# Performance work log

Measured on AMD Instinct MI355X. Metric: run time of the kernel, lower is better.

## Reference

```python
import jax, jax.numpy as jnp
import numpy as np


def _conv(x, w, padding):
    # x: NCHW, w: OIHW
    return jax.lax.conv_general_dilated(
        x, w, window_strides=(1, 1), padding=padding,
        dimension_numbers=('NCHW', 'OIHW', 'NCHW'))


def setup_inputs() -> dict:
    key = jax.random.key(0)
    ks = jax.random.split(key, 4)
    B, Cin, H, W = 128, 1024, 14, 14
    planes, expansion = 256, 4
    x = jax.random.normal(ks[0], (B, Cin, H, W), dtype=jnp.float32)
    # conv weights (layouts are fully dense since rho=0.0)
    w1 = jax.random.normal(ks[1], (planes, Cin, 1, 1), dtype=jnp.float32) * 0.02
    w2 = jax.random.normal(ks[2], (planes, planes, 3, 3), dtype=jnp.float32) * 0.02
    w3 = jax.random.normal(ks[3], (planes * expansion, planes, 1, 1), dtype=jnp.float32) * 0.02
    # Fixup scalar biases / scale
    z = jnp.zeros((1,), dtype=jnp.float32)
    return {
        'x': x, 'w1': w1, 'w2': w2, 'w3': w3,
        'bias1b': z, 'bias2a': z, 'bias2b': z, 'bias3a': z, 'bias3b': z,
        'rscale': jnp.ones((1,), dtype=jnp.float32), 'rbias': z,
    }


def reference(x, w1, w2, w3, bias1b, bias2a, bias2b, bias3a, bias3b, rscale, rbias):
    # conv1(x) + bias1b  (1x1, fused output bias)
    out = _conv(x, w1, 'VALID') + bias1b[0]
    # conv2(out + bias2a) + bias2b  (3x3, pad 1, fused input+output bias)
    out = _conv(out + bias2a[0], w2, 'SAME') + bias2b[0]
    # conv3(out + bias3a) + bias3b  (1x1)
    out = _conv(out + bias3a[0], w3, 'VALID') + bias3b[0]
    # fused scale + bias + residual ReLU: relu(out*rscale + rbias + identity)
    return jax.nn.relu(out * rscale[0] + rbias[0] + x)
```

## Files before the change

### kernel.cpp

```cpp
#include <hip/hip_runtime.h>
#include <stdint.h>

typedef __bf16 bf16x8 __attribute__((ext_vector_type(8)));
typedef float f32x4 __attribute__((ext_vector_type(4)));
typedef unsigned short u16;

__device__ __forceinline__ u16 f2bf(float f){
  uint32_t u = __float_as_uint(f);
  u = (u + 0x7fffu + ((u >> 16) & 1u)) >> 16;
  return (u16)u;
}
__device__ __forceinline__ float bf2f(u16 v){
  return __uint_as_float(((uint32_t)v) << 16);
}
__device__ __forceinline__ void gl_lds16(const void* g, void* l){
  __builtin_amdgcn_global_load_lds((const __attribute__((address_space(1))) void*)g,
                                   (__attribute__((address_space(3))) void*)l, 16, 0, 0);
}

__global__ __launch_bounds__(256) void prep_w(
    const float* __restrict__ w1, const float* __restrict__ w2,
    const float* __restrict__ w3, u16* __restrict__ wb1, u16* __restrict__ wb2,
    u16* __restrict__ wb3){
  int bid = blockIdx.x, t = threadIdx.x;
  if (bid < 1024){
    int i = bid*256 + t; wb1[i] = f2bf(w1[i]);
  } else if (bid < 3328){
    int i = (bid-1024)*256 + t;
    int o = i / 2304, r = i - o*2304, kq = r >> 8, c = r & 255;
    wb2[i] = f2bf(w2[((size_t)o*256 + c)*9 + kq]);
  } else {
    int i = (bid-3328)*256 + t; wb3[i] = f2bf(w3[i]);
  }
}

__global__ __launch_bounds__(256) void transform_x(const float* __restrict__ x,
                                                   u16* __restrict__ xp0){
  __shared__ float lds[64*201];
  const int b = blockIdx.y, c0 = blockIdx.x*64, t = threadIdx.x;
  const float4* src = (const float4*)x + (size_t)b*50176 + (size_t)c0*49;
  #pragma unroll
  for (int r = 0; r < 13; ++r){
    int q = r*256 + t;
    if (q < 3136){
      unsigned c = (unsigned)q / 49u, f = (unsigned)q - c*49u;
      float4 v = src[q];
      float* d = &lds[c*201 + f*4];
      d[0]=v.x; d[1]=v.y; d[2]=v.z; d[3]=v.w;
    }
  }
  __syncthreads();
  const int c4 = (t & 15)*4, pg = t >> 4;
  #pragma unroll
  for (int r = 0; r < 13; ++r){
    int p = r*16 + pg;
    if (p < 196){
      ushort4 pk;
      ((u16*)&pk)[0] = f2bf(lds[(c4+0)*201 + p]);
      ((u16*)&pk)[1] = f2bf(lds[(c4+1)*201 + p]);
      ((u16*)&pk)[2] = f2bf(lds[(c4+2)*201 + p]);
      ((u16*)&pk)[3] = f2bf(lds[(c4+3)*201 + p]);
      *(ushort4*)&xp0[((size_t)b*196 + p)*1024 + c0 + c4] = pk;
    }
  }
}

__global__ __launch_bounds__(512, 1) void gemm1_conv(
    const u16* __restrict__ A, const u16* __restrict__ B, u16* __restrict__ O,
    const float* __restrict__ s0, const float* __restrict__ s1){
  extern __shared__ char lds[];
  const int t = threadIdx.x, lane = t & 63, w = t >> 6;
  const int wm = (w >> 2) * 64, wn = (w & 3) * 64;
  const int b = blockIdx.x & 127, m0 = (blockIdx.x >> 7) * 128;
  f32x4 acc[4][4] = {};

  uint32_t aoff[2], boff[4];
  #pragma unroll
  for (int i = 0; i < 2; ++i){
    int gl = i*512 + t, row = gl >> 3, ss = gl & 7;
    aoff[i] = (uint32_t)(m0 + row)*2048 + ((ss ^ (row & 7)) << 4);
  }
  #pragma unroll
  for (int i = 0; i < 4; ++i){
    int gl = i*512 + t, row = gl >> 3, ss = gl & 7;
    int y = row >> 4, x = row & 15;
    int p = ((unsigned)(y-1) < 14u && (unsigned)(x-1) < 14u) ? (y-1)*14 + (x-1) : 0;
    boff[i] = ((uint32_t)b*196 + p)*2048 + ((ss ^ (row & 7)) << 4);
  }

  auto stage = [&](int buf, int kc){
    char* Ab = lds + buf*16384;
    char* Bb = lds + 32768 + buf*32768;
    #pragma unroll
    for (int i = 0; i < 2; ++i)
      gl_lds16((const char*)A + aoff[i] + kc*128, Ab + (i*512 + t)*16);
    #pragma unroll
    for (int i = 0; i < 4; ++i)
      gl_lds16((const char*)B + boff[i] + kc*128, Bb + (i*512 + t)*16);
  };
  auto compute = [&](int buf){
    char* Ab = lds + buf*16384;
    char* Bb = lds + 32768 + buf*32768;
    #pragma unroll
    for (int h = 0; h < 2; ++h){
      bf16x8 af[4], bfr[4];
      #pragma unroll
      for (int i = 0; i < 4; ++i){
        int row = wm + i*16 + (lane & 15);
        af[i] = *(const bf16x8*)(Ab + row*128 + (((h*4 + (lane>>4)) ^ (row & 7)) << 4));
      }
      #pragma unroll
      for (int j = 0; j < 4; ++j){
        int row = wn + j*16 + (lane & 15);
        bfr[j] = *(const bf16x8*)(Bb + row*128 + (((h*4 + (lane>>4)) ^ (row & 7)) << 4));
      }
      #pragma unroll
      for (int i = 0; i < 4; ++i)
        #pragma unroll
        for (int j = 0; j < 4; ++j)
          acc[i][j] = __builtin_amdgcn_mfma_f32_16x16x32_bf16(af[i], bfr[j], acc[i][j], 0, 0, 0);
    }
  };

  stage(0, 0);
  __syncthreads();
  #pragma unroll
  for (int kc = 0; kc < 16; ++kc){
    if (kc < 15) stage((kc+1) & 1, kc+1);
    compute(kc & 1);
    __syncthreads();
  }

  float badd = s0[0] + s1[0];
  #pragma unroll
  for (int i = 0; i < 4; ++i){
    int o = m0 + wm + i*16 + ((lane >> 4) << 2);
    #pragma unroll
    for (int j = 0; j < 4; ++j){
      int n = wn + j*16 + (lane & 15);
      int y = n >> 4, x = n & 15;
      bool real = ((unsigned)(y-1) < 14u) && ((unsigned)(x-1) < 14u);
      ushort4 pk;
      #pragma unroll
      for (int q = 0; q < 4; ++q)
        ((u16*)&pk)[q] = real ? f2bf(acc[i][j][q] + badd) : (u16)0;
      *(ushort4*)(O + ((size_t)b*256 + n)*256 + o) = pk;
    }
  }
}

__global__ __launch_bounds__(512, 1) void gemm2_conv(
    const u16* __restrict__ A, const u16* __restrict__ B, u16* __restrict__ O,
    const float* __restrict__ s0, const float* __restrict__ s1){
  extern __shared__ char lds[];
  const int t = threadIdx.x, lane = t & 63, w = t >> 6;
  const int wm = (w >> 2) * 64, wn = (w & 3) * 64;
  const int b = blockIdx.x & 127, m0 = (blockIdx.x >> 7) * 128;
  f32x4 acc[4][4] = {};

  uint32_t aoff[2], boff[5];
  #pragma unroll
  for (int i = 0; i < 2; ++i){
    int gl = i*512 + t, row = gl >> 3, ss = gl & 7;
    aoff[i] = (uint32_t)(m0 + row)*4608 + ((ss ^ (row & 7)) << 4);
  }
  #pragma unroll
  for (int i = 0; i < 5; ++i){
    int gl = i*512 + t, row = gl >> 3, ss = gl & 7;
    int pos = row - 18;
    pos = pos < 0 ? 0 : (pos > 255 ? 255 : pos);
    boff[i] = ((uint32_t)b*256 + pos)*512 + ((ss ^ (row & 7)) << 4);
  }

  auto stageA = [&](int buf, int kq, int kc){
    char* Ab = lds + buf*16384;
    int off = kq*512 + kc*128;
    #pragma unroll
    for (int i = 0; i < 2; ++i)
      gl_lds16((const char*)A + aoff[i] + off, Ab + (i*512 + t)*16);
  };
  auto stageB = [&](int buf, int kc){
    char* Bb = lds + 32768 + buf*37376;
    #pragma unroll
    for (int i = 0; i < 5; ++i){
      int gl = i*512 + t;
      if (gl < 2336) gl_lds16((const char*)B + boff[i] + kc*128, Bb + gl*16);
    }
  };
  auto compute = [&](int ab, int bb, int shift){
    char* Ab = lds + ab*16384;
    char* Bb = lds + 32768 + bb*37376;
    #pragma unroll
    for (int h = 0; h < 2; ++h){
      bf16x8 af[4], bfr[4];
      #pragma unroll
      for (int i = 0; i < 4; ++i){
        int row = wm + i*16 + (lane & 15);
        af[i] = *(const bf16x8*)(Ab + row*128 + (((h*4 + (lane>>4)) ^ (row & 7)) << 4));
      }
      #pragma unroll
      for (int j = 0; j < 4; ++j){
        int row = 18 + wn + j*16 + (lane & 15) + shift;
        bfr[j] = *(const bf16x8*)(Bb + row*128 + (((h*4 + (lane>>4)) ^ (row & 7)) << 4));
      }
      #pragma unroll
      for (int i = 0; i < 4; ++i)
        #pragma unroll
        for (int j = 0; j < 4; ++j)
          acc[i][j] = __builtin_amdgcn_mfma_f32_16x16x32_bf16(af[i], bfr[j], acc[i][j], 0, 0, 0);
    }
  };

  stageB(0, 0); stageA(0, 0, 0);
  __syncthreads();
  int ab = 0, bbuf = 0;
  #pragma unroll
  for (int kc = 0; kc < 4; ++kc){
    #pragma unroll
    for (int kq = 0; kq < 9; ++kq){
      if (kq < 8) stageA(ab ^ 1, kq + 1, kc);
      else if (kc < 3){ stageB(bbuf ^ 1, kc + 1); stageA(ab ^ 1, 0, kc + 1); }
      compute(ab, bbuf, (kq/3 - 1)*16 + (kq%3) - 1);
      __syncthreads();
      ab ^= 1;
      if (kq == 8) bbuf ^= 1;
    }
  }

  float badd = s0[0] + s1[0];
  #pragma unroll
  for (int i = 0; i < 4; ++i){
    int o = m0 + wm + i*16 + ((lane >> 4) << 2);
    #pragma unroll
    for (int j = 0; j < 4; ++j){
      int n = wn + j*16 + (lane & 15);
      int y = n >> 4, x = n & 15;
      if (((unsigned)(y-1) < 14u) && ((unsigned)(x-1) < 14u)){
        int p = (y-1)*14 + (x-1);
        ushort4 pk;
        #pragma unroll
        for (int q = 0; q < 4; ++q) ((u16*)&pk)[q] = f2bf(acc[i][j][q] + badd);
        *(ushort4*)(O + ((size_t)b*196 + p)*256 + o) = pk;
      }
    }
  }
}

__global__ __launch_bounds__(256, 4) void gemm3_conv(
    const u16* __restrict__ A, const u16* __restrict__ B, const u16* __restrict__ xresb,
    float* __restrict__ Of32, const float* __restrict__ s0, const float* __restrict__ s1,
    const float* __restrict__ s2){
  __shared__ char lds[33792];
  const int t = threadIdx.x, lane = t & 63, w = t >> 6;
  const int wm = (w >> 1) * 64, wn = (w & 1) * 64;
  const int orig = blockIdx.x;
  const int bid  = (orig & 7) * ((int)gridDim.x >> 3) + (orig >> 3);
  const int n0 = (bid >> 3) * 128, m0 = (bid & 7) * 128;
  f32x4 acc[4][4] = {};

  uint32_t aoff[4], boff[4];
  #pragma unroll
  for (int i = 0; i < 4; ++i){
    int gl = i*256 + t, row = gl >> 3, ss = gl & 7;
    int xo = (ss ^ (row & 7)) << 4;
    aoff[i] = (uint32_t)(m0 + row)*512 + xo;
    boff[i] = (uint32_t)(n0 + row)*512 + xo;
  }

  auto stage = [&](int s){
    char* Ab = lds;
    char* Bb = lds + 16384;
    #pragma unroll
    for (int i = 0; i < 4; ++i){
      gl_lds16((const char*)A + aoff[i] + s*128, Ab + (i*256 + t)*16);
      gl_lds16((const char*)B + boff[i] + s*128, Bb + (i*256 + t)*16);
    }
  };
  auto compute = [&](){
    char* Ab = lds;
    char* Bb = lds + 16384;
    #pragma unroll
    for (int h = 0; h < 2; ++h){
      bf16x8 af[4], bfr[4];
      #pragma unroll
      for (int i = 0; i < 4; ++i){
        int row = wm + i*16 + (lane & 15);
        af[i] = *(const bf16x8*)(Ab + row*128 + (((h*4 + (lane>>4)) ^ (row & 7)) << 4));
      }
      #pragma unroll
      for (int j = 0; j < 4; ++j){
        int row = wn + j*16 + (lane & 15);
        bfr[j] = *(const bf16x8*)(Bb + row*128 + (((h*4 + (lane>>4)) ^ (row & 7)) << 4));
      }
      #pragma unroll
      for (int i = 0; i < 4; ++i)
        #pragma unroll
        for (int j = 0; j < 4; ++j)
          acc[i][j] = __builtin_amdgcn_mfma_f32_16x16x32_bf16(af[i], bfr[j], acc[i][j], 0, 0, 0);
    }
  };

  #pragma unroll
  for (int s = 0; s < 4; ++s){
    if (s) __syncthreads();
    stage(s);
    __syncthreads();
    compute();
  }

  float b3 = s0[0], rs = s1[0], rbv = s2[0];
  float* ldsF = (float*)lds;
  #pragma unroll
  for (int pass = 0; pass < 2; ++pass){
    __syncthreads();
    if ((wm >> 6) == pass){
      #pragma unroll
      for (int i = 0; i < 4; ++i){
        int rb = i*16 + ((lane >> 4) << 2);
        #pragma unroll
        for (int j = 0; j < 4; ++j){
          int col = wn + j*16 + (lane & 15);
          #pragma unroll
          for (int q = 0; q < 4; ++q) ldsF[(rb + q)*132 + col] = acc[i][j][q];
        }
      }
    }
    __syncthreads();
    #pragma unroll
    for (int r = 0; r < 8; ++r){
      int row = (w << 4) + ((lane >> 5) << 3) + r;
      int n4  = (lane & 31) << 2;
      float4 v = *(float4*)&ldsF[row*132 + n4];
      uint32_t n = n0 + n4;
      uint32_t b = n / 196u, p = n - b*196u;
      int o = m0 + pass*64 + row;
      size_t base = ((size_t)b*1024 + o)*196 + p;
      const u16* xr = xresb + (size_t)n*1024 + o;
      float4 ov;
      ov.x = fmaxf((v.x + b3)*rs + rbv + bf2f(xr[0]),    0.f);
      ov.y = fmaxf((v.y + b3)*rs + rbv + bf2f(xr[1024]), 0.f);
      ov.z = fmaxf((v.z + b3)*rs + rbv + bf2f(xr[2048]), 0.f);
      ov.w = fmaxf((v.w + b3)*rs + rbv + bf2f(xr[3072]), 0.f);
      *(float4*)&Of32[base] = ov;
    }
  }
}

extern "C" void kernel_launch(void* const* d_in, const int* in_sizes, int n_in,
                              void* d_out, int out_size, void* d_ws, size_t ws_size,
                              hipStream_t stream){
  (void)in_sizes; (void)n_in; (void)out_size; (void)ws_size;
  const float* x   = (const float*)d_in[0];
  const float* w1  = (const float*)d_in[1];
  const float* w2  = (const float*)d_in[2];
  const float* w3  = (const float*)d_in[3];
  const float* b1b = (const float*)d_in[4];
  const float* b2a = (const float*)d_in[5];
  const float* b2b = (const float*)d_in[6];
  const float* b3a = (const float*)d_in[7];
  const float* b3b = (const float*)d_in[8];
  const float* rsc = (const float*)d_in[9];
  const float* rbi = (const float*)d_in[10];

  char* ws  = (char*)d_ws;
  u16*  xp1 = (u16*)ws;
  u16*  xp2 = (u16*)(ws + 16777216);
  u16*  xp0 = (u16*)(ws + 29622272);
  u16*  wb1 = (u16*)(ws + 81002496);
  u16*  wb2 = (u16*)(ws + 81526784);
  u16*  wb3 = (u16*)(ws + 82706432);

  prep_w     <<<dim3(4352),   256, 0, stream>>>(w1, w2, w3, wb1, wb2, wb3);
  transform_x<<<dim3(16,128), 256, 0, stream>>>(x, xp0);

  gemm1_conv<<<dim3(256),  512,  98304, stream>>>(wb1, xp0, xp1, b1b, b2a);
  gemm2_conv<<<dim3(256),  512, 107520, stream>>>(wb2, xp1, xp2, b2b, b3a);
  gemm3_conv<<<dim3(1568), 256,      0, stream>>>(wb3, xp2, xp0, (float*)d_out, b3b, rsc, rbi);
}
```

Baseline: 320.0 us.

## Fuse conv1 and conv2 into one kernel keeping intermediate in LDS

Merges the 1x1 conv1 GEMM and the 3x3 conv2 GEMM into a single kernel. Each block handles half an image's padded rows plus a halo, computes all 256 conv1 channels, and stores the result as bf16 in LDS. conv2 then reads its shifted input straight from LDS instead of a global intermediate, and streams the conv2 weights through registers into LDS. This removes the intermediate global round trip and one launch, but recomputes the halo rows and uses register staging with two barriers per step for the weights. The fused kernel also needs a larger LDS footprint (128 KB per block).

```diff
diff --git a/kernel.cpp b/kernel.cpp
--- a/kernel.cpp
+++ b/kernel.cpp
@@ -65,184 +65,196 @@
   }
 }
 
-__global__ __launch_bounds__(512, 1) void gemm1_conv(
-    const u16* __restrict__ A, const u16* __restrict__ B, u16* __restrict__ O,
-    const float* __restrict__ s0, const float* __restrict__ s1){
+__global__ __launch_bounds__(512, 2) void gemm12_conv(
+    const u16* __restrict__ wb1, const u16* __restrict__ wb2,
+    const u16* __restrict__ xp0, u16* __restrict__ xp2,
+    const float* __restrict__ b1b, const float* __restrict__ b2a,
+    const float* __restrict__ b2b, const float* __restrict__ b3a)
+{
   extern __shared__ char lds[];
   const int t = threadIdx.x, lane = t & 63, w = t >> 6;
-  const int wm = (w >> 2) * 64, wn = (w & 3) * 64;
-  const int b = blockIdx.x & 127, m0 = (blockIdx.x >> 7) * 128;
-  f32x4 acc[4][4] = {};
-
-  uint32_t aoff[2], boff[4];
-  #pragma unroll
-  for (int i = 0; i < 2; ++i){
-    int gl = i*512 + t, row = gl >> 3, ss = gl & 7;
-    aoff[i] = (uint32_t)(m0 + row)*2048 + ((ss ^ (row & 7)) << 4);
-  }
+  const int wm  = (w >> 2) * 64;
+  const int wn1 = (w & 3) * 48;
+  const int wn2 = (w & 3) * 32;
+  const int b = blockIdx.x >> 1, half = blockIdx.x & 1;
+  const int g0 = half*128 - 32;
+
+  uint32_t a1off[4], b0off[3];
   #pragma unroll
   for (int i = 0; i < 4; ++i){
     int gl = i*512 + t, row = gl >> 3, ss = gl & 7;
-    int y = row >> 4, x = row & 15;
-    int p = ((unsigned)(y-1) < 14u && (unsigned)(x-1) < 14u) ? (y-1)*14 + (x-1) : 0;
-    boff[i] = ((uint32_t)b*196 + p)*2048 + ((ss ^ (row & 7)) << 4);
-  }
-
-  auto stage = [&](int buf, int kc){
-    char* Ab = lds + buf*16384;
-    char* Bb = lds + 32768 + buf*32768;
-    #pragma unroll
-    for (int i = 0; i < 2; ++i)
-      gl_lds16((const char*)A + aoff[i] + kc*128, Ab + (i*512 + t)*16);
+    a1off[i] = (uint32_t)row*2048 + ((ss ^ (row & 7)) << 4);
+  }
+  #pragma unroll
+  for (int i = 0; i < 3; ++i){
+    int gl = i*512 + t, row = gl >> 3, ss = gl & 7;
+    int P = g0 + row, y = P >> 4, x = P & 15;
+    bool valid = ((unsigned)P < 256u) && ((unsigned)(y-1) < 14u) && ((unsigned)(x-1) < 14u);
+    int preal = valid ? (y-1)*14 + (x-1) : 0;
+    b0off[i] = ((uint32_t)b*196 + preal)*2048 + ((ss ^ (row & 7)) << 4);
+  }
+
+  f32x4 acc1[2][4][3] = {};
+
+  auto stage1 = [&](int buf, int s){
+    char* B0 = lds + buf*24576;
+    char* A1 = lds + 49152 + buf*32768;
     #pragma unroll
     for (int i = 0; i < 4; ++i)
-      gl_lds16((const char*)B + boff[i] + kc*128, Bb + (i*512 + t)*16);
-  };
-  auto compute = [&](int buf){
-    char* Ab = lds + buf*16384;
-    char* Bb = lds + 32768 + buf*32768;
+      gl_lds16((const char*)wb1 + a1off[i] + s*128, A1 + (i*512 + t)*16);
+    #pragma unroll
+    for (int i = 0; i < 3; ++i)
+      gl_lds16((const char*)xp0 + b0off[i] + s*128, B0 + (i*512 + t)*16);
+  };
+  auto compute1 = [&](int buf){
+    char* B0 = lds + buf*24576;
+    char* A1 = lds + 49152 + buf*32768;
     #pragma unroll
     for (int h = 0; h < 2; ++h){
-      bf16x8 af[4], bfr[4];
+      bf16x8 af[2][4], bf[3];
+      #pragma unroll
+      for (int p = 0; p < 2; ++p)
+        #pragma unroll
+        for (int i = 0; i < 4; ++i){
+          int row = p*128 + wm + i*16 + (lane & 15);
+          af[p][i] = *(const bf16x8*)(A1 + row*128 + (((h*4 + (lane>>4)) ^ (row & 7)) << 4));
+        }
+      #pragma unroll
+      for (int j = 0; j < 3; ++j){
+        int row = wn1 + j*16 + (lane & 15);
+        bf[j] = *(const bf16x8*)(B0 + row*128 + (((h*4 + (lane>>4)) ^ (row & 7)) << 4));
+      }
+      #pragma unroll
+      for (int p = 0; p < 2; ++p)
+        #pragma unroll
+        for (int i = 0; i < 4; ++i)
+          #pragma unroll
+          for (int j = 0; j < 3; ++j)
+            acc1[p][i][j] = __builtin_amdgcn_mfma_f32_16x16x32_bf16(af[p][i], bf[j], acc1[p][i][j], 0, 0, 0);
+    }
+  };
+
+  stage1(0, 0);
+  __syncthreads();
+  for (int s = 0; s < 16; ++s){
+    if (s < 15) stage1((s+1) & 1, s+1);
+    compute1(s & 1);
+    __syncthreads();
+  }
+
+  {
+    float badd1 = b1b[0] + b2a[0];
+    #pragma unroll
+    for (int p = 0; p < 2; ++p)
       #pragma unroll
       for (int i = 0; i < 4; ++i){
-        int row = wm + i*16 + (lane & 15);
-        af[i] = *(const bf16x8*)(Ab + row*128 + (((h*4 + (lane>>4)) ^ (row & 7)) << 4));
-      }
-      #pragma unroll
-      for (int j = 0; j < 4; ++j){
-        int row = wn + j*16 + (lane & 15);
-        bfr[j] = *(const bf16x8*)(Bb + row*128 + (((h*4 + (lane>>4)) ^ (row & 7)) << 4));
-      }
-      #pragma unroll
-      for (int i = 0; i < 4; ++i)
-        #pragma unroll
-        for (int j = 0; j < 4; ++j)
-          acc[i][j] = __builtin_amdgcn_mfma_f32_16x16x32_bf16(af[i], bfr[j], acc[i][j], 0, 0, 0);
-    }
-  };
-
-  stage(0, 0);
+        int o = p*128 + wm + i*16 + ((lane >> 4) << 2);
+        int go = o >> 3;
+        #pragma unroll
+        for (int j = 0; j < 3; ++j){
+          int ni = wn1 + j*16 + (lane & 15);
+          int P = g0 + ni, y = P >> 4, x = P & 15;
+          bool valid = ((unsigned)P < 256u) && ((unsigned)(y-1) < 14u) && ((unsigned)(x-1) < 14u);
+          ushort4 pk;
+          #pragma unroll
+          for (int q = 0; q < 4; ++q)
+            ((u16*)&pk)[q] = valid ? f2bf(acc1[p][i][j][q] + badd1) : (u16)0;
+          int gs = (go & 24) | ((go & 7) ^ (ni & 7));
+          *(ushort4*)(lds + ni*512 + (gs << 4) + (o & 7)*2) = pk;
+        }
+      }
+  }
   __syncthreads();
-  #pragma unroll
-  for (int kc = 0; kc < 16; ++kc){
-    if (kc < 15) stage((kc+1) & 1, kc+1);
-    compute(kc & 1);
-    __syncthreads();
-  }
-
-  float badd = s0[0] + s1[0];
-  #pragma unroll
-  for (int i = 0; i < 4; ++i){
-    int o = m0 + wm + i*16 + ((lane >> 4) << 2);
-    #pragma unroll
-    for (int j = 0; j < 4; ++j){
-      int n = wn + j*16 + (lane & 15);
-      int y = n >> 4, x = n & 15;
-      bool real = ((unsigned)(y-1) < 14u) && ((unsigned)(x-1) < 14u);
-      ushort4 pk;
-      #pragma unroll
-      for (int q = 0; q < 4; ++q)
-        ((u16*)&pk)[q] = real ? f2bf(acc[i][j][q] + badd) : (u16)0;
-      *(ushort4*)(O + ((size_t)b*256 + n)*256 + o) = pk;
-    }
-  }
-}
-
-__global__ __launch_bounds__(512, 1) void gemm2_conv(
-    const u16* __restrict__ A, const u16* __restrict__ B, u16* __restrict__ O,
-    const float* __restrict__ s0, const float* __restrict__ s1){
-  extern __shared__ char lds[];
-  const int t = threadIdx.x, lane = t & 63, w = t >> 6;
-  const int wm = (w >> 2) * 64, wn = (w & 3) * 64;
-  const int b = blockIdx.x & 127, m0 = (blockIdx.x >> 7) * 128;
-  f32x4 acc[4][4] = {};
-
-  uint32_t aoff[2], boff[5];
-  #pragma unroll
-  for (int i = 0; i < 2; ++i){
-    int gl = i*512 + t, row = gl >> 3, ss = gl & 7;
-    aoff[i] = (uint32_t)(m0 + row)*4608 + ((ss ^ (row & 7)) << 4);
-  }
-  #pragma unroll
-  for (int i = 0; i < 5; ++i){
-    int gl = i*512 + t, row = gl >> 3, ss = gl & 7;
-    int pos = row - 18;
-    pos = pos < 0 ? 0 : (pos > 255 ? 255 : pos);
-    boff[i] = ((uint32_t)b*256 + pos)*512 + ((ss ^ (row & 7)) << 4);
-  }
-
-  auto stageA = [&](int buf, int kq, int kc){
-    char* Ab = lds + buf*16384;
-    int off = kq*512 + kc*128;
-    #pragma unroll
-    for (int i = 0; i < 2; ++i)
-      gl_lds16((const char*)A + aoff[i] + off, Ab + (i*512 + t)*16);
-  };
-  auto stageB = [&](int buf, int kc){
-    char* Bb = lds + 32768 + buf*37376;
-    #pragma unroll
-    for (int i = 0; i < 5; ++i){
-      int gl = i*512 + t;
-      if (gl < 2336) gl_lds16((const char*)B + boff[i] + kc*128, Bb + gl*16);
-    }
-  };
-  auto compute = [&](int ab, int bb, int shift){
-    char* Ab = lds + ab*16384;
-    char* Bb = lds + 32768 + bb*37376;
-    #pragma unroll
-    for (int h = 0; h < 2; ++h){
-      bf16x8 af[4], bfr[4];
+
+  char* A2 = lds + 98304;
+  uint32_t a2base[4];
+  #pragma unroll
+  for (int r = 0; r < 4; ++r){
+    int gl = r*512 + t, row = gl >> 3, ss = gl & 7;
+    a2base[r] = (uint32_t)row*4608 + ((ss ^ (row & 7)) << 4);
+  }
+  uint4 ar[4];
+  auto loadA2 = [&](int kq, int kc){
+    uint32_t off = (uint32_t)kq*512 + (uint32_t)kc*128;
+    #pragma unroll
+    for (int r = 0; r < 4; ++r)
+      ar[r] = *(const uint4*)((const char*)wb2 + a2base[r] + off);
+  };
+  auto writeA2 = [&](){
+    #pragma unroll
+    for (int r = 0; r < 4; ++r)
+      *(uint4*)(A2 + (r*512 + t)*16) = ar[r];
+  };
+
+  f32x4 acc2[2][4][2] = {};
+
+  loadA2(0, 0);
+  writeA2();
+  __syncthreads();
+
+  #pragma unroll
+  for (int kq = 0; kq < 9; ++kq){
+    const int dy = kq/3 - 1, dx = kq%3 - 1;
+    const int shift = dy*16 + dx;
+    #pragma unroll
+    for (int kc = 0; kc < 4; ++kc){
+      bool more = !(kq == 8 && kc == 3);
+      if (more){
+        int nkq = (kc == 3) ? kq + 1 : kq;
+        int nkc = (kc == 3) ? 0 : kc + 1;
+        loadA2(nkq, nkc);
+      }
+      #pragma unroll
+      for (int h = 0; h < 2; ++h){
+        bf16x8 af[2][4], bf[2];
+        #pragma unroll
+        for (int p = 0; p < 2; ++p)
+          #pragma unroll
+          for (int i = 0; i < 4; ++i){
+            int row = p*128 + wm + i*16 + (lane & 15);
+            af[p][i] = *(const bf16x8*)(A2 + row*128 + (((h*4 + (lane>>4)) ^ (row & 7)) << 4));
+          }
+        #pragma unroll
+        for (int j = 0; j < 2; ++j){
+          int row = 32 + wn2 + j*16 + (lane & 15) + shift;
+          int gk = kc*8 + h*4 + (lane >> 4);
+          int gs = (gk & 24) | ((gk & 7) ^ (row & 7));
+          bf[j] = *(const bf16x8*)(lds + row*512 + (gs << 4));
+        }
+        #pragma unroll
+        for (int p = 0; p < 2; ++p)
+          #pragma unroll
+          for (int i = 0; i < 4; ++i)
+            #pragma unroll
+            for (int j = 0; j < 2; ++j)
+              acc2[p][i][j] = __builtin_amdgcn_mfma_f32_16x16x32_bf16(af[p][i], bf[j], acc2[p][i][j], 0, 0, 0);
+      }
+      __syncthreads();
+      if (more) writeA2();
+      __syncthreads();
+    }
+  }
+
+  {
+    float badd2 = b2b[0] + b3a[0];
+    #pragma unroll
+    for (int p = 0; p < 2; ++p)
       #pragma unroll
       for (int i = 0; i < 4; ++i){
-        int row = wm + i*16 + (lane & 15);
-        af[i] = *(const bf16x8*)(Ab + row*128 + (((h*4 + (lane>>4)) ^ (row & 7)) << 4));
-      }
-      #pragma unroll
-      for (int j = 0; j < 4; ++j){
-        int row = 18 + wn + j*16 + (lane & 15) + shift;
-        bfr[j] = *(const bf16x8*)(Bb + row*128 + (((h*4 + (lane>>4)) ^ (row & 7)) << 4));
-      }
-      #pragma unroll
-      for (int i = 0; i < 4; ++i)
-        #pragma unroll
-        for (int j = 0; j < 4; ++j)
-          acc[i][j] = __builtin_amdgcn_mfma_f32_16x16x32_bf16(af[i], bfr[j], acc[i][j], 0, 0, 0);
-    }
-  };
-
-  stageB(0, 0); stageA(0, 0, 0);
-  __syncthreads();
-  int ab = 0, bbuf = 0;
-  #pragma unroll
-  for (int kc = 0; kc < 4; ++kc){
-    #pragma unroll
-    for (int kq = 0; kq < 9; ++kq){
-      if (kq < 8) stageA(ab ^ 1, kq + 1, kc);
-      else if (kc < 3){ stageB(bbuf ^ 1, kc + 1); stageA(ab ^ 1, 0, kc + 1); }
-      compute(ab, bbuf, (kq/3 - 1)*16 + (kq%3) - 1);
-      __syncthreads();
-      ab ^= 1;
-      if (kq == 8) bbuf ^= 1;
-    }
-  }
-
-  float badd = s0[0] + s1[0];
-  #pragma unroll
-  for (int i = 0; i < 4; ++i){
-    int o = m0 + wm + i*16 + ((lane >> 4) << 2);
-    #pragma unroll
-    for (int j = 0; j < 4; ++j){
-      int n = wn + j*16 + (lane & 15);
-      int y = n >> 4, x = n & 15;
-      if (((unsigned)(y-1) < 14u) && ((unsigned)(x-1) < 14u)){
-        int p = (y-1)*14 + (x-1);
-        ushort4 pk;
-        #pragma unroll
-        for (int q = 0; q < 4; ++q) ((u16*)&pk)[q] = f2bf(acc[i][j][q] + badd);
-        *(ushort4*)(O + ((size_t)b*196 + p)*256 + o) = pk;
-      }
-    }
+        int o = p*128 + wm + i*16 + ((lane >> 4) << 2);
+        #pragma unroll
+        for (int j = 0; j < 2; ++j){
+          int no = wn2 + j*16 + (lane & 15);
+          int P = half*128 + no, y = P >> 4, x = P & 15;
+          if (((unsigned)(y-1) < 14u) && ((unsigned)(x-1) < 14u)){
+            int preal = (y-1)*14 + (x-1);
+            ushort4 pk;
+            #pragma unroll
+            for (int q = 0; q < 4; ++q) ((u16*)&pk)[q] = f2bf(acc2[p][i][j][q] + badd2);
+            *(ushort4*)(xp2 + ((size_t)b*196 + preal)*256 + o) = pk;
+          }
+        }
+      }
   }
 }
 
@@ -363,7 +375,6 @@
   const float* rbi = (const float*)d_in[10];
 
   char* ws  = (char*)d_ws;
-  u16*  xp1 = (u16*)ws;
   u16*  xp2 = (u16*)(ws + 16777216);
   u16*  xp0 = (u16*)(ws + 29622272);
   u16*  wb1 = (u16*)(ws + 81002496);
@@ -373,7 +384,6 @@
   prep_w     <<<dim3(4352),   256, 0, stream>>>(w1, w2, w3, wb1, wb2, wb3);
   transform_x<<<dim3(16,128), 256, 0, stream>>>(x, xp0);
 
-  gemm1_conv<<<dim3(256),  512,  98304, stream>>>(wb1, xp0, xp1, b1b, b2a);
-  gemm2_conv<<<dim3(256),  512, 107520, stream>>>(wb2, xp1, xp2, b2b, b3a);
-  gemm3_conv<<<dim3(1568), 256,      0, stream>>>(wb3, xp2, xp0, (float*)d_out, b3b, rsc, rbi);
-}
+  gemm12_conv<<<dim3(256),  512, 131072, stream>>>(wb1, wb2, xp0, xp2, b1b, b2a, b2b, b3a);
+  gemm3_conv <<<dim3(1568), 256,      0, stream>>>(wb3, xp2, xp0, (float*)d_out, b3b, rsc, rbi);
+}
```

Result: slower. 394.5 us (+23.3%).
